# Performance work log

Hardware: AMD Instinct MI355X
Metric: run time of the kernel (lower is better)

The kernel has to match this reference:

```python
import jax, jax.numpy as jnp
import numpy as np

B, N, E = 128, 49, 2048        # batch, num image regions, encoder_dim
EMB, D, V = 512, 512, 12000    # embed_size, decoder_dim, vocab_size
TCAP = 22                      # caption length (T = TCAP-1 decode steps)


def _lin(key, out_dim, in_dim):
    kw, kb = jax.random.split(key)
    s = 1.0 / np.sqrt(in_dim)
    return (jax.random.uniform(kw, (out_dim, in_dim), jnp.float32, -s, s),
            jax.random.uniform(kb, (out_dim,), jnp.float32, -s, s))


def setup_inputs() -> dict:
    key = jax.random.key(0)
    ks = jax.random.split(key, 12)
    features = jax.random.normal(ks[0], (B, N, E), jnp.float32)
    captions = jax.random.randint(ks[1], (B, TCAP), 0, V)
    embedding = jax.random.normal(ks[2], (V, EMB), jnp.float32) * 0.05
    Wa_w, Wa_b = _lin(ks[3], D, E)
    Ua_w, Ua_b = _lin(ks[4], D, D)
    Va_w, Va_b = _lin(ks[5], 1, D)
    W_ih, b_ih = _lin(ks[6], 4 * D, E + EMB)
    W_hh, b_hh = _lin(ks[7], 4 * D, D)
    ih_w, ih_b = _lin(ks[8], D, E)
    ic_w, ic_b = _lin(ks[9], D, E)
    fc_w, fc_b = _lin(ks[10], V, D)
    return dict(features=features, captions=captions, embedding=embedding,
                Wa_w=Wa_w, Wa_b=Wa_b, Ua_w=Ua_w, Ua_b=Ua_b, Va_w=Va_w, Va_b=Va_b,
                W_ih=W_ih, W_hh=W_hh, b_ih=b_ih, b_hh=b_hh,
                ih_w=ih_w, ih_b=ih_b, ic_w=ic_w, ic_b=ic_b,
                fc_w=fc_w, fc_b=fc_b)


def reference(features, captions, embedding, Wa_w, Wa_b, Ua_w, Ua_b, Va_w, Va_b,
              W_ih, W_hh, b_ih, b_hh, ih_w, ih_b, ic_w, ic_b, fc_w, fc_b):
    caps = captions[:, :-1]                      # [B, T]
    embeds = embedding[caps]                     # [B, T, EMB]
    mean_f = features.mean(axis=1)               # [B, E]
    h0 = mean_f @ ih_w.T + ih_b                  # [B, D]
    c0 = mean_f @ ic_w.T + ic_b
    # W_a(features) is time-invariant -> hoist out of the recurrence
    f_proj = jnp.einsum('bne,de->bnd', features, Wa_w) + Wa_b  # [B, N, D]

    def step(carry, word_embed):
        h, c = carry
        # additive attention
        h_proj = h @ Ua_w.T + Ua_b                          # [B, D]
        comb = jnp.tanh(f_proj + h_proj[:, None, :])        # [B, N, D]
        scores = (comb @ Va_w.T + Va_b)[..., 0]             # [B, N]
        scores = jax.nn.softmax(scores, axis=1)
        context = jnp.einsum('bne,bn->be', features, scores)  # [B, E]
        # LSTMCell (dropout is identity in eval)
        x = jnp.concatenate([context, word_embed], axis=1)  # [B, E+EMB]
        gates = x @ W_ih.T + b_ih + h @ W_hh.T + b_hh       # [B, 4D]
        i, f, g, o = jnp.split(gates, 4, axis=1)
        i, f, o = jax.nn.sigmoid(i), jax.nn.sigmoid(f), jax.nn.sigmoid(o)
        g = jnp.tanh(g)
        c2 = f * c + i * g
        h2 = o * jnp.tanh(c2)
        out = h2 @ fc_w.T + fc_b                            # [B, V]
        return (h2, c2), (scores, out)

    _, (weights, preds) = jax.lax.scan(step, (h0, c0), jnp.swapaxes(embeds, 0, 1))
    return jnp.swapaxes(weights, 0, 1), jnp.swapaxes(preds, 0, 1)
```

## Files before the change

kernel.cpp:

```cpp
#include <hip/hip_runtime.h>
#include <math.h>
#include <stdint.h>

#define BATCH 128
#define NF 49
#define EDIM 2048
#define EMBD 512
#define DDIM 512
#define VOC 12000
#define VOCP 12032
#define TT 21
#define G4 2048
#define UWN 2560

typedef __bf16 bf16x8 __attribute__((ext_vector_type(8)));
typedef float f32x4 __attribute__((ext_vector_type(4)));
typedef unsigned short ushortx8 __attribute__((ext_vector_type(8)));
typedef unsigned short u16;

union U8 { ushortx8 u; bf16x8 b; };

__device__ __forceinline__ u16 bf16_rne(float x) {
    union { float f; unsigned u; } v; v.f = x;
    unsigned r = v.u + 0x7fffu + ((v.u >> 16) & 1u);
    return (u16)(r >> 16);
}
__device__ __forceinline__ float bf16_to_f(u16 h) {
    union { unsigned u; float f; } v; v.u = ((unsigned)h) << 16;
    return v.f;
}
__device__ __forceinline__ float sigmoidf(float x) { return 1.f / (1.f + expf(-x)); }

__device__ __forceinline__ void gload16(const void* g, void* l) {
    auto gp = reinterpret_cast<const __attribute__((address_space(1))) unsigned int*>(
        reinterpret_cast<uintptr_t>(g));
    auto lp = reinterpret_cast<__attribute__((address_space(3))) unsigned int*>(
        reinterpret_cast<uintptr_t>(l));
    __builtin_amdgcn_global_load_lds(gp, lp, 16, 0, 0);
}

__global__ __launch_bounds__(256) void gemm_bf16s2(
    const u16* __restrict__ Ahi, const u16* __restrict__ Alo, int lda,
    const u16* __restrict__ Whi, const u16* __restrict__ Wlo, int ldw,
    float* __restrict__ C1, int ldc1,
    float* __restrict__ C2, int ldc2, int nsplit,
    const float* __restrict__ bias,
    int Nn, int K)
{
    __shared__ u16 Ah[128 * 32];
    __shared__ u16 Al[128 * 32];
    __shared__ u16 Wh[128 * 32];
    __shared__ u16 Wl[128 * 32];

    const int nbx = gridDim.x;
    const int nwg = nbx * gridDim.y;
    const int orig = blockIdx.y * nbx + blockIdx.x;
    const int q = nwg >> 3, r = nwg & 7;
    const int xcd = orig & 7, pos = orig >> 3;
    const int swz = (xcd < r ? xcd * (q + 1) : r * (q + 1) + (xcd - r) * q) + pos;
    const int by = swz / nbx, bx = swz - by * nbx;

    const int bm = by * 128;
    const int bn = bx * 128;
    const int tid = threadIdx.x;
    const int lane = tid & 63;
    const int wid = tid >> 6;
    const int wr = (wid >> 1) * 64;
    const int wc = (wid & 1) * 64;

    const int srow = wid * 32 + (lane >> 2);
    const int sslot = (lane & 3) ^ ((lane >> 2) & 3);
    const u16* a_src = Ahi + (size_t)(bm + srow) * lda + sslot * 8;
    const u16* al_src = Alo + (size_t)(bm + srow) * lda + sslot * 8;
    const u16* w_src = Whi + (size_t)(bn + srow) * ldw + sslot * 8;
    const u16* wl_src = Wlo + (size_t)(bn + srow) * ldw + sslot * 8;
    const int lds_base = (wid * 32) * 32;

    const int fr = lane & 15;
    const int ksl = lane >> 4;
    const int rsl = (ksl ^ (fr & 3)) * 8;

    f32x4 acc[4][4] = {};

    for (int k0 = 0; k0 < K; k0 += 32) {
        #pragma unroll
        for (int cch = 0; cch < 2; ++cch) {
            const size_t go = (size_t)cch * 16 * lda + k0;
            const size_t gw = (size_t)cch * 16 * ldw + k0;
            const int lo = lds_base + cch * 16 * 32;
            gload16(a_src + go, &Ah[lo]);
            gload16(al_src + go, &Al[lo]);
            gload16(w_src + gw, &Wh[lo]);
            gload16(wl_src + gw, &Wl[lo]);
        }
        __syncthreads();

        bf16x8 av_h[4], av_l[4], wv_h[4], wv_l[4];
        #pragma unroll
        for (int m = 0; m < 4; ++m) {
            int ar = wr + m * 16 + fr;
            av_h[m] = *(const bf16x8*)&Ah[ar * 32 + rsl];
            av_l[m] = *(const bf16x8*)&Al[ar * 32 + rsl];
        }
        #pragma unroll
        for (int n = 0; n < 4; ++n) {
            int wrw = wc + n * 16 + fr;
            wv_h[n] = *(const bf16x8*)&Wh[wrw * 32 + rsl];
            wv_l[n] = *(const bf16x8*)&Wl[wrw * 32 + rsl];
        }
        #pragma unroll
        for (int m = 0; m < 4; ++m)
            #pragma unroll
            for (int n = 0; n < 4; ++n) {
                acc[m][n] = __builtin_amdgcn_mfma_f32_16x16x32_bf16(av_h[m], wv_h[n], acc[m][n], 0, 0, 0);
                acc[m][n] = __builtin_amdgcn_mfma_f32_16x16x32_bf16(av_h[m], wv_l[n], acc[m][n], 0, 0, 0);
                acc[m][n] = __builtin_amdgcn_mfma_f32_16x16x32_bf16(av_l[m], wv_h[n], acc[m][n], 0, 0, 0);
            }
        __syncthreads();
    }

    #pragma unroll
    for (int n = 0; n < 4; ++n) {
        int col = bn + wc + n * 16 + (lane & 15);
        if (col >= Nn) continue;
        float bv = bias ? bias[col] : 0.f;
        float* Cd; int ldcd; int cc;
        if (col < nsplit) { Cd = C1; ldcd = ldc1; cc = col; }
        else              { Cd = C2; ldcd = ldc2; cc = col - nsplit; }
        #pragma unroll
        for (int m = 0; m < 4; ++m) {
            int row0 = bm + wr + m * 16 + (lane >> 4) * 4;
            #pragma unroll
            for (int rg = 0; rg < 4; ++rg)
                Cd[(size_t)(row0 + rg) * ldcd + cc] = acc[m][n][rg] + bv;
        }
    }
}

__global__ __launch_bounds__(256) void small_mfma_gemm2(
    const float* __restrict__ A, int lda,
    const u16* __restrict__ Whi,
    const u16* __restrict__ Wlo,
    int K,
    const float* __restrict__ bias,
    float* __restrict__ C1, int ldc1,
    float* __restrict__ C2, int ldc2, int nsplit)
{
    const int tid = threadIdx.x;
    const int wave = tid >> 6;
    const int lane = tid & 63;
    const int g = blockIdx.x * 4 + wave;
    const int mt = g & 7;
    const int nt = g >> 3;
    const int fr = lane & 15;
    const int ksl = lane >> 4;

    const float* arow = A + (size_t)(mt * 16 + fr) * lda + ksl * 8;
    const u16* bhi = Whi + (size_t)(nt * 16 + fr) * K + ksl * 8;
    const u16* blo = Wlo + (size_t)(nt * 16 + fr) * K + ksl * 8;

    f32x4 acc = {};
    for (int k0 = 0; k0 < K; k0 += 32) {
        float4 f0 = *(const float4*)(arow + k0);
        float4 f1 = *(const float4*)(arow + k0 + 4);
        U8 ah, al;
        float fv[8] = {f0.x, f0.y, f0.z, f0.w, f1.x, f1.y, f1.z, f1.w};
        #pragma unroll
        for (int j = 0; j < 8; ++j) {
            u16 hh = bf16_rne(fv[j]);
            ah.u[j] = hh;
            al.u[j] = bf16_rne(fv[j] - bf16_to_f(hh));
        }
        U8 bh, bl;
        bh.u = *(const ushortx8*)(bhi + k0);
        bl.u = *(const ushortx8*)(blo + k0);
        acc = __builtin_amdgcn_mfma_f32_16x16x32_bf16(ah.b, bh.b, acc, 0, 0, 0);
        acc = __builtin_amdgcn_mfma_f32_16x16x32_bf16(ah.b, bl.b, acc, 0, 0, 0);
        acc = __builtin_amdgcn_mfma_f32_16x16x32_bf16(al.b, bh.b, acc, 0, 0, 0);
    }

    const int n = nt * 16 + (lane & 15);
    const int m0 = mt * 16 + (lane >> 4) * 4;
    const float bv = bias ? bias[n] : 0.f;
    float* Cd; int ldcd; int cc;
    if (n < nsplit) { Cd = C1; ldcd = ldc1; cc = n; }
    else            { Cd = C2; ldcd = ldc2; cc = n - nsplit; }
    #pragma unroll
    for (int rg = 0; rg < 4; ++rg)
        Cd[(size_t)(m0 + rg) * ldcd + cc] = acc[rg] + bv;
}

#define MS_C0 2097152
#define MS_C1 7340032
#define MS_C2 8388608
#define MS_C3 9699328
#define MS_C4 22544384
#define MS_C5 22552576

__global__ __launch_bounds__(256) void mega_split_kernel(
    const float* __restrict__ ih_w, const float* __restrict__ ic_w,
    const float* __restrict__ Wa_w, const float* __restrict__ W_ih,
    const float* __restrict__ Ua_w, const float* __restrict__ W_hh,
    const float* __restrict__ features,
    const float* __restrict__ b_ih, const float* __restrict__ b_hh,
    const float* __restrict__ Ua_b, const float* __restrict__ Wa_b,
    const float* __restrict__ ih_b, const float* __restrict__ ic_b,
    u16* __restrict__ T_hi, u16* __restrict__ T_lo,
    u16* __restrict__ WaWf_hi, u16* __restrict__ WaWf_lo,
    u16* __restrict__ We_hi, u16* __restrict__ We_lo,
    u16* __restrict__ UW_hi, u16* __restrict__ UW_lo,
    u16* __restrict__ feat_hi, u16* __restrict__ feat_lo,
    float* __restrict__ bsum, float* __restrict__ biascat,
    float* __restrict__ bias_fp, float* __restrict__ bias_hc)
{
    const int idx = blockIdx.x * 256 + threadIdx.x;
    float v; u16* hi; u16* lo; int j;

    if (idx < MS_C0) {
        j = idx; int r = j >> 11, k = j & 2047;
        v = (r < 512) ? ih_w[(size_t)r * 2048 + k] : ic_w[(size_t)(r - 512) * 2048 + k];
        hi = T_hi; lo = T_lo;
    } else if (idx < MS_C1) {
        j = idx - MS_C0; int r = j >> 11, k = j & 2047;
        v = (r < 512) ? Wa_w[(size_t)r * 2048 + k] : W_ih[(size_t)(r - 512) * 2560 + k];
        hi = WaWf_hi; lo = WaWf_lo;
    } else if (idx < MS_C2) {
        j = idx - MS_C1; int r = j >> 9, k = j & 511;
        v = W_ih[(size_t)r * 2560 + 2048 + k];
        hi = We_hi; lo = We_lo;
    } else if (idx < MS_C3) {
        j = idx - MS_C2; int r = j >> 9, k = j & 511;
        v = (r < 512) ? Ua_w[(size_t)r * 512 + k] : W_hh[(size_t)(r - 512) * 512 + k];
        hi = UW_hi; lo = UW_lo;
    } else if (idx < MS_C4) {
        j = idx - MS_C3;
        v = features[j];
        hi = feat_hi; lo = feat_lo;
    } else {
        j = idx - MS_C4;
        if (j < 2048)       bsum[j] = b_ih[j] + b_hh[j];
        else if (j < 4608)  { int jj = j - 2048; biascat[jj] = (jj < 512) ? Ua_b[jj] : 0.f; }
        else if (j < 7168)  { int jj = j - 4608; bias_fp[jj] = (jj < 512) ? Wa_b[jj] : 0.f; }
        else                { int jj = j - 7168; bias_hc[jj] = (jj < 512) ? ih_b[jj] : ic_b[jj - 512]; }
        return;
    }
    u16 h = bf16_rne(v);
    hi[j] = h;
    lo[j] = bf16_rne(v - bf16_to_f(h));
}

__global__ __launch_bounds__(256) void split_mat_kernel(
    const float* __restrict__ src, int srcld, int cols, int rows, int rows_pad,
    u16* __restrict__ hi, u16* __restrict__ lo)
{
    int idx = blockIdx.x * 256 + threadIdx.x;
    if (idx >= rows_pad * cols) return;
    int r = idx / cols, k = idx - r * cols;
    float v = (r < rows) ? src[(size_t)r * srcld + k] : 0.f;
    u16 h = bf16_rne(v);
    hi[idx] = h;
    lo[idx] = bf16_rne(v - bf16_to_f(h));
}

__global__ __launch_bounds__(256) void mean_feat_kernel(const float* __restrict__ features,
                                                        float* __restrict__ mean_f)
{
    int idx = blockIdx.x * 256 + threadIdx.x;
    int b = idx >> 11, e = idx & 2047;
    float s = 0.f;
    for (int n = 0; n < NF; ++n)
        s += features[((size_t)(b * NF + n)) * EDIM + e];
    mean_f[idx] = s * (1.0f / NF);
}

__global__ __launch_bounds__(256) void gather_embed_split_kernel(const int* __restrict__ captions,
                                                                 const float* __restrict__ embedding,
                                                                 u16* __restrict__ ehi,
                                                                 u16* __restrict__ elo)
{
    int idx = blockIdx.x * 256 + threadIdx.x;
    int m = idx >> 9;
    int j = idx & 511;
    int b = m / TT, t = m - b * TT;
    int word = captions[b * (TT + 1) + t];
    float v = embedding[(size_t)word * EMBD + j];
    u16 h = bf16_rne(v);
    ehi[idx] = h;
    elo[idx] = bf16_rne(v - bf16_to_f(h));
}

__global__ __launch_bounds__(512) void fused_step3_kernel(
    const float* __restrict__ f_proj,
    const float* __restrict__ hp_g,
    const float* __restrict__ Va_w,
    const float* __restrict__ Va_b,
    const float* __restrict__ F_ih,
    const float* __restrict__ E_ih,
    float* __restrict__ h,
    float* __restrict__ c,
    u16* __restrict__ H_hi, u16* __restrict__ H_lo,
    float* __restrict__ out_w,
    int t)
{
    const int b  = blockIdx.x >> 1;
    const int dh = blockIdx.x & 1;
    const int tid = threadIdx.x;
    const int wid = tid >> 6;
    const int lane = tid & 63;
    __shared__ float s[64];
    __shared__ float pb[1024];
    __shared__ float gs2[1024];

    const float* hp = hp_g + (size_t)b * UWN;
    for (int n = wid; n < NF; n += 8) {
        const float* fp = f_proj + ((size_t)(b * NF + n)) * DDIM;
        float sum = 0.f;
        for (int d = lane; d < DDIM; d += 64)
            sum += Va_w[d] * tanhf(fp[d] + hp[d]);
        for (int off = 32; off; off >>= 1) sum += __shfl_down(sum, off);
        if (lane == 0) s[n] = sum + Va_b[0];
    }
    __syncthreads();
    if (tid < 64) {
        float v = (lane < NF) ? s[lane] : -1e30f;
        float mx = v;
        for (int off = 32; off; off >>= 1) mx = fmaxf(mx, __shfl_xor(mx, off));
        float e = (lane < NF) ? expf(v - mx) : 0.f;
        float sm = e;
        for (int off = 32; off; off >>= 1) sm += __shfl_xor(sm, off);
        float p = e / sm;
        s[lane] = (lane < NF) ? p : 0.f;
        if (dh == 0 && lane < NF)
            out_w[((size_t)b * TT + t) * NF + lane] = p;
    }
    __syncthreads();

    const int cg = tid & 255;
    const int nh = tid >> 8;
    const int q  = cg >> 6;
    const int dl = (cg & 63) * 4;
    const int gcol = q * DDIM + dh * 256 + dl;
    const float* fib = F_ih + (size_t)b * NF * G4 + gcol;

    float4 a;
    if (nh == 0) {
        a = *(const float4*)(hp + DDIM + gcol);
        float4 e4 = *(const float4*)(E_ih + ((size_t)b * TT + t) * G4 + gcol);
        a.x += e4.x; a.y += e4.y; a.z += e4.z; a.w += e4.w;
    } else {
        a = make_float4(0.f, 0.f, 0.f, 0.f);
    }
    const int n0 = nh ? 25 : 0;
    const int n1 = nh ? NF : 25;
    #pragma unroll 5
    for (int n = n0; n < n1; ++n) {
        float w = s[n];
        float4 f4 = *(const float4*)(fib + (size_t)n * G4);
        a.x += w * f4.x; a.y += w * f4.y; a.z += w * f4.z; a.w += w * f4.w;
    }
    if (nh == 1) *(float4*)&pb[cg * 4] = a;
    __syncthreads();
    if (nh == 0) {
        float4 p4 = *(const float4*)&pb[cg * 4];
        a.x += p4.x; a.y += p4.y; a.z += p4.z; a.w += p4.w;
        *(float4*)&gs2[cg * 4] = a;
    }
    __syncthreads();

    if (tid < 64) {
        const int d   = dh * 256 + tid * 4;
        const int idx = b * DDIM + d;
        float4 iv4 = *(const float4*)&gs2[(0 * 64 + tid) * 4];
        float4 fv4 = *(const float4*)&gs2[(1 * 64 + tid) * 4];
        float4 gv4 = *(const float4*)&gs2[(2 * 64 + tid) * 4];
        float4 ov4 = *(const float4*)&gs2[(3 * 64 + tid) * 4];
        float4 cold = *(const float4*)(c + idx);
        float ci[4] = {cold.x, cold.y, cold.z, cold.w};
        float ii[4] = {iv4.x, iv4.y, iv4.z, iv4.w};
        float ff[4] = {fv4.x, fv4.y, fv4.z, fv4.w};
        float gg[4] = {gv4.x, gv4.y, gv4.z, gv4.w};
        float oo[4] = {ov4.x, ov4.y, ov4.z, ov4.w};
        float co[4], ho[4];
        u16 hh4[4], hl4[4];
        #pragma unroll
        for (int k = 0; k < 4; ++k) {
            float iv = sigmoidf(ii[k]);
            float fv = sigmoidf(ff[k]);
            float gv = tanhf(gg[k]);
            float ov = sigmoidf(oo[k]);
            float c2 = fv * ci[k] + iv * gv;
            float h2 = ov * tanhf(c2);
            co[k] = c2; ho[k] = h2;
            hh4[k] = bf16_rne(h2);
            hl4[k] = bf16_rne(h2 - bf16_to_f(hh4[k]));
        }
        *(float4*)(c + idx) = make_float4(co[0], co[1], co[2], co[3]);
        *(float4*)(h + idx) = make_float4(ho[0], ho[1], ho[2], ho[3]);
        size_t hix = ((size_t)b * TT + t) * DDIM + d;
        *(ushort4*)(H_hi + hix) = make_ushort4(hh4[0], hh4[1], hh4[2], hh4[3]);
        *(ushort4*)(H_lo + hix) = make_ushort4(hl4[0], hl4[1], hl4[2], hl4[3]);
    }
}

extern "C" void kernel_launch(void* const* d_in, const int* in_sizes, int n_in,
                              void* d_out, int out_size, void* d_ws, size_t ws_size,
                              hipStream_t stream)
{
    const float* features = (const float*)d_in[0];
    const int*   captions = (const int*)d_in[1];
    const float* embedding= (const float*)d_in[2];
    const float* Wa_w = (const float*)d_in[3];
    const float* Wa_b = (const float*)d_in[4];
    const float* Ua_w = (const float*)d_in[5];
    const float* Ua_b = (const float*)d_in[6];
    const float* Va_w = (const float*)d_in[7];
    const float* Va_b = (const float*)d_in[8];
    const float* W_ih = (const float*)d_in[9];
    const float* W_hh = (const float*)d_in[10];
    const float* b_ih = (const float*)d_in[11];
    const float* b_hh = (const float*)d_in[12];
    const float* ih_w = (const float*)d_in[13];
    const float* ih_b = (const float*)d_in[14];
    const float* ic_w = (const float*)d_in[15];
    const float* ic_b = (const float*)d_in[16];
    const float* fc_w = (const float*)d_in[17];
    const float* fc_b = (const float*)d_in[18];

    float* out_w = (float*)d_out;
    float* out_p = out_w + (size_t)BATCH * TT * NF;

    float* ws = (float*)d_ws;
    size_t off = 0;
    auto alloc = [&](size_t n) { float* p = ws + off; off += n; return p; };

    float* f_proj  = alloc(3211264);
    float* F_ih    = alloc(12845056);
    float* E_ih    = alloc(5505024);
    float* hp_g    = alloc(327680);
    float* mean_f  = alloc(262144);
    float* h       = alloc(65536);
    float* c       = alloc(65536);
    float* bsum    = alloc(2048);
    float* biascat = alloc(2560);
    float* bias_fp = alloc(2560);
    float* bias_hc = alloc(1024);
    u16* feat_hi = (u16*)alloc(6422528);
    u16* feat_lo = (u16*)alloc(6422528);
    u16* emb_hi  = (u16*)alloc(688128);
    u16* emb_lo  = (u16*)alloc(688128);
    u16* H_hi    = (u16*)alloc(688128);
    u16* H_lo    = (u16*)alloc(688128);
    u16* WaWf_hi = (u16*)alloc(2621440);
    u16* WaWf_lo = (u16*)alloc(2621440);
    u16* We_hi   = (u16*)alloc(524288);
    u16* We_lo   = (u16*)alloc(524288);
    u16* UW_hi   = (u16*)alloc(655360);
    u16* UW_lo   = (u16*)alloc(655360);
    u16* fcw_hi  = (u16*)alloc(3080192);
    u16* fcw_lo  = (u16*)alloc(3080192);

    u16* T_hi = fcw_hi;
    u16* T_lo = fcw_lo;

    hipLaunchKernelGGL(mega_split_kernel, dim3(MS_C5 / 256), dim3(256), 0, stream,
                       ih_w, ic_w, Wa_w, W_ih, Ua_w, W_hh, features,
                       b_ih, b_hh, Ua_b, Wa_b, ih_b, ic_b,
                       T_hi, T_lo, WaWf_hi, WaWf_lo, We_hi, We_lo,
                       UW_hi, UW_lo, feat_hi, feat_lo,
                       bsum, biascat, bias_fp, bias_hc);
    hipLaunchKernelGGL(mean_feat_kernel, dim3(BATCH * EDIM / 256), dim3(256), 0, stream,
                       features, mean_f);
    hipLaunchKernelGGL(small_mfma_gemm2, dim3(1024 / 8), dim3(256), 0, stream,
                       mean_f, EDIM, T_hi, T_lo, EDIM, bias_hc,
                       h, DDIM, c, DDIM, DDIM);
    hipLaunchKernelGGL(split_mat_kernel, dim3((VOCP * DDIM + 255) / 256), dim3(256), 0, stream,
                       fc_w, DDIM, DDIM, VOC, VOCP, fcw_hi, fcw_lo);
    hipLaunchKernelGGL(gather_embed_split_kernel, dim3(BATCH * TT * EMBD / 256), dim3(256), 0, stream,
                       captions, embedding, emb_hi, emb_lo);

    {
        dim3 grid(UWN / 128, BATCH * NF / 128);
        hipLaunchKernelGGL(gemm_bf16s2, grid, dim3(256), 0, stream,
                           feat_hi, feat_lo, EDIM, WaWf_hi, WaWf_lo, EDIM,
                           f_proj, DDIM, F_ih, G4, DDIM, bias_fp, UWN, EDIM);
    }
    {
        dim3 grid(G4 / 128, BATCH * TT / 128);
        hipLaunchKernelGGL(gemm_bf16s2, grid, dim3(256), 0, stream,
                           emb_hi, emb_lo, EMBD, We_hi, We_lo, EMBD,
                           E_ih, G4, E_ih, G4, G4, bsum, G4, EMBD);
    }

    for (int t = 0; t < TT; ++t) {
        hipLaunchKernelGGL(small_mfma_gemm2, dim3(UWN / 8), dim3(256), 0, stream,
                           h, DDIM, UW_hi, UW_lo, DDIM, biascat,
                           hp_g, UWN, hp_g, UWN, UWN);
        hipLaunchKernelGGL(fused_step3_kernel, dim3(BATCH * 2), dim3(512), 0, stream,
                           f_proj, hp_g, Va_w, Va_b, F_ih, E_ih, h, c,
                           H_hi, H_lo, out_w, t);
    }

    {
        dim3 grid(VOCP / 128, BATCH * TT / 128);
        hipLaunchKernelGGL(gemm_bf16s2, grid, dim3(256), 0, stream,
                           H_hi, H_lo, DDIM, fcw_hi, fcw_lo, DDIM,
                           out_p, VOC, out_p, VOC, VOCP, fc_b, VOC, DDIM);
    }
}
```

Baseline: 1.499 ms.

## Split per-step LSTM kernel into four column quarters and fold embed gather into split kernel

The per-step fused attention+LSTM kernel now uses four blocks per batch row instead of two. Each block handles 128 of the hidden columns, and the 49-region context reduction is spread over four thread groups, so the grid grows to 512 blocks. The cost is that each block now recomputes the attention scores and softmax redundantly. Separately, the caption embedding gather and its bf16 hi/lo split are merged into the mega split kernel, removing one launch.

Result: no change. 1.510 ms (+0.8%).

```diff
diff --git a/kernel.cpp b/kernel.cpp
--- a/kernel.cpp
+++ b/kernel.cpp
@@ -195,13 +195,15 @@
 #define MS_C2 8388608
 #define MS_C3 9699328
 #define MS_C4 22544384
-#define MS_C5 22552576
+#define MS_C5 23920640
+#define MS_C6 23928832
 
 __global__ __launch_bounds__(256) void mega_split_kernel(
     const float* __restrict__ ih_w, const float* __restrict__ ic_w,
     const float* __restrict__ Wa_w, const float* __restrict__ W_ih,
     const float* __restrict__ Ua_w, const float* __restrict__ W_hh,
     const float* __restrict__ features,
+    const int* __restrict__ captions, const float* __restrict__ embedding,
     const float* __restrict__ b_ih, const float* __restrict__ b_hh,
     const float* __restrict__ Ua_b, const float* __restrict__ Wa_b,
     const float* __restrict__ ih_b, const float* __restrict__ ic_b,
@@ -210,6 +212,7 @@
     u16* __restrict__ We_hi, u16* __restrict__ We_lo,
     u16* __restrict__ UW_hi, u16* __restrict__ UW_lo,
     u16* __restrict__ feat_hi, u16* __restrict__ feat_lo,
+    u16* __restrict__ emb_hi, u16* __restrict__ emb_lo,
     float* __restrict__ bsum, float* __restrict__ biascat,
     float* __restrict__ bias_fp, float* __restrict__ bias_hc)
 {
@@ -236,8 +239,14 @@
         j = idx - MS_C3;
         v = features[j];
         hi = feat_hi; lo = feat_lo;
+    } else if (idx < MS_C5) {
+        j = idx - MS_C4; int m = j >> 9, k = j & 511;
+        int b = m / TT, t = m - b * TT;
+        int word = captions[b * (TT + 1) + t];
+        v = embedding[(size_t)word * EMBD + k];
+        hi = emb_hi; lo = emb_lo;
     } else {
-        j = idx - MS_C4;
+        j = idx - MS_C5;
         if (j < 2048)       bsum[j] = b_ih[j] + b_hh[j];
         else if (j < 4608)  { int jj = j - 2048; biascat[jj] = (jj < 512) ? Ua_b[jj] : 0.f; }
         else if (j < 7168)  { int jj = j - 4608; bias_fp[jj] = (jj < 512) ? Wa_b[jj] : 0.f; }
@@ -273,23 +282,7 @@
     mean_f[idx] = s * (1.0f / NF);
 }
 
-__global__ __launch_bounds__(256) void gather_embed_split_kernel(const int* __restrict__ captions,
-                                                                 const float* __restrict__ embedding,
-                                                                 u16* __restrict__ ehi,
-                                                                 u16* __restrict__ elo)
-{
-    int idx = blockIdx.x * 256 + threadIdx.x;
-    int m = idx >> 9;
-    int j = idx & 511;
-    int b = m / TT, t = m - b * TT;
-    int word = captions[b * (TT + 1) + t];
-    float v = embedding[(size_t)word * EMBD + j];
-    u16 h = bf16_rne(v);
-    ehi[idx] = h;
-    elo[idx] = bf16_rne(v - bf16_to_f(h));
-}
-
-__global__ __launch_bounds__(512) void fused_step3_kernel(
+__global__ __launch_bounds__(512) void fused_step4_kernel(
     const float* __restrict__ f_proj,
     const float* __restrict__ hp_g,
     const float* __restrict__ Va_w,
@@ -302,14 +295,14 @@
     float* __restrict__ out_w,
     int t)
 {
-    const int b  = blockIdx.x >> 1;
-    const int dh = blockIdx.x & 1;
+    const int b  = blockIdx.x >> 2;
+    const int qd = blockIdx.x & 3;
     const int tid = threadIdx.x;
     const int wid = tid >> 6;
     const int lane = tid & 63;
     __shared__ float s[64];
-    __shared__ float pb[1024];
-    __shared__ float gs2[1024];
+    __shared__ float pb[3][512];
+    __shared__ float gs2[512];
 
     const float* hp = hp_g + (size_t)b * UWN;
     for (int n = wid; n < NF; n += 8) {
@@ -330,16 +323,16 @@
         for (int off = 32; off; off >>= 1) sm += __shfl_xor(sm, off);
         float p = e / sm;
         s[lane] = (lane < NF) ? p : 0.f;
-        if (dh == 0 && lane < NF)
+        if (qd == 0 && lane < NF)
             out_w[((size_t)b * TT + t) * NF + lane] = p;
     }
     __syncthreads();
 
-    const int cg = tid & 255;
-    const int nh = tid >> 8;
-    const int q  = cg >> 6;
-    const int dl = (cg & 63) * 4;
-    const int gcol = q * DDIM + dh * 256 + dl;
+    const int cg = tid & 127;
+    const int nh = tid >> 7;
+    const int q  = cg >> 5;
+    const int dl = (cg & 31) * 4;
+    const int gcol = q * DDIM + qd * 128 + dl;
     const float* fib = F_ih + (size_t)b * NF * G4 + gcol;
 
     float4 a;
@@ -350,30 +343,35 @@
     } else {
         a = make_float4(0.f, 0.f, 0.f, 0.f);
     }
-    const int n0 = nh ? 25 : 0;
-    const int n1 = nh ? NF : 25;
-    #pragma unroll 5
+    const int n0 = nh ? (12 * nh + 1) : 0;
+    const int n1 = 12 * nh + 13;
+    #pragma unroll 4
     for (int n = n0; n < n1; ++n) {
         float w = s[n];
         float4 f4 = *(const float4*)(fib + (size_t)n * G4);
         a.x += w * f4.x; a.y += w * f4.y; a.z += w * f4.z; a.w += w * f4.w;
     }
-    if (nh == 1) *(float4*)&pb[cg * 4] = a;
+    if (nh) *(float4*)&pb[nh - 1][cg * 4] = a;
     __syncthreads();
     if (nh == 0) {
-        float4 p4 = *(const float4*)&pb[cg * 4];
-        a.x += p4.x; a.y += p4.y; a.z += p4.z; a.w += p4.w;
+        float4 p0 = *(const float4*)&pb[0][cg * 4];
+        float4 p1 = *(const float4*)&pb[1][cg * 4];
+        float4 p2 = *(const float4*)&pb[2][cg * 4];
+        a.x += p0.x + p1.x + p2.x;
+        a.y += p0.y + p1.y + p2.y;
+        a.z += p0.z + p1.z + p2.z;
+        a.w += p0.w + p1.w + p2.w;
         *(float4*)&gs2[cg * 4] = a;
     }
     __syncthreads();
 
-    if (tid < 64) {
-        const int d   = dh * 256 + tid * 4;
+    if (tid < 32) {
+        const int d   = qd * 128 + tid * 4;
         const int idx = b * DDIM + d;
-        float4 iv4 = *(const float4*)&gs2[(0 * 64 + tid) * 4];
-        float4 fv4 = *(const float4*)&gs2[(1 * 64 + tid) * 4];
-        float4 gv4 = *(const float4*)&gs2[(2 * 64 + tid) * 4];
-        float4 ov4 = *(const float4*)&gs2[(3 * 64 + tid) * 4];
+        float4 iv4 = *(const float4*)&gs2[(0 * 32 + tid) * 4];
+        float4 fv4 = *(const float4*)&gs2[(1 * 32 + tid) * 4];
+        float4 gv4 = *(const float4*)&gs2[(2 * 32 + tid) * 4];
+        float4 ov4 = *(const float4*)&gs2[(3 * 32 + tid) * 4];
         float4 cold = *(const float4*)(c + idx);
         float ci[4] = {cold.x, cold.y, cold.z, cold.w};
         float ii[4] = {iv4.x, iv4.y, iv4.z, iv4.w};
@@ -462,11 +460,12 @@
     u16* T_hi = fcw_hi;
     u16* T_lo = fcw_lo;
 
-    hipLaunchKernelGGL(mega_split_kernel, dim3(MS_C5 / 256), dim3(256), 0, stream,
+    hipLaunchKernelGGL(mega_split_kernel, dim3(MS_C6 / 256), dim3(256), 0, stream,
                        ih_w, ic_w, Wa_w, W_ih, Ua_w, W_hh, features,
+                       captions, embedding,
                        b_ih, b_hh, Ua_b, Wa_b, ih_b, ic_b,
                        T_hi, T_lo, WaWf_hi, WaWf_lo, We_hi, We_lo,
-                       UW_hi, UW_lo, feat_hi, feat_lo,
+                       UW_hi, UW_lo, feat_hi, feat_lo, emb_hi, emb_lo,
                        bsum, biascat, bias_fp, bias_hc);
     hipLaunchKernelGGL(mean_feat_kernel, dim3(BATCH * EDIM / 256), dim3(256), 0, stream,
                        features, mean_f);
@@ -475,8 +474,6 @@
                        h, DDIM, c, DDIM, DDIM);
     hipLaunchKernelGGL(split_mat_kernel, dim3((VOCP * DDIM + 255) / 256), dim3(256), 0, stream,
                        fc_w, DDIM, DDIM, VOC, VOCP, fcw_hi, fcw_lo);
-    hipLaunchKernelGGL(gather_embed_split_kernel, dim3(BATCH * TT * EMBD / 256), dim3(256), 0, stream,
-                       captions, embedding, emb_hi, emb_lo);
 
     {
         dim3 grid(UWN / 128, BATCH * NF / 128);
@@ -495,7 +492,7 @@
         hipLaunchKernelGGL(small_mfma_gemm2, dim3(UWN / 8), dim3(256), 0, stream,
                            h, DDIM, UW_hi, UW_lo, DDIM, biascat,
                            hp_g, UWN, hp_g, UWN, UWN);
-        hipLaunchKernelGGL(fused_step3_kernel, dim3(BATCH * 2), dim3(512), 0, stream,
+        hipLaunchKernelGGL(fused_step4_kernel, dim3(BATCH * 4), dim3(512), 0, stream,
                            f_proj, hp_g, Va_w, Va_b, F_ih, E_ih, h, c,
                            H_hi, H_lo, out_w, t);
     }
```
